# Kernel tuning notes

Hardware: AMD Instinct MI355X
Metric: run time of the kernel (lower is better)

The kernel has to match this reference:

```python
import jax, jax.numpy as jnp
import numpy as np

N_ENT, N_USR, C, E, NNZ, NREL, NHOPS = 150000, 60000, 64, 1000000, 1000000, 10, 2
EPS = 1e-12  # torch F.normalize default eps


def setup_inputs() -> dict:
    key = jax.random.key(0)
    ks = jax.random.split(key, 8)
    return {
        "user_emb": jax.random.normal(ks[0], (N_USR, C), dtype=jnp.float32),
        "entity_emb": jax.random.normal(ks[1], (N_ENT, C), dtype=jnp.float32),
        "weight": jax.random.normal(ks[2], (NREL - 1, C), dtype=jnp.float32) * 0.1,  # xavier-ish
        "inter_vals": jax.random.uniform(ks[3], (NNZ,), dtype=jnp.float32),
        "edge_index": jax.random.randint(ks[4], (2, E), 0, N_ENT),
        "edge_type": jax.random.randint(ks[5], (E,), 0, NREL - 1),
        "inter_rows": jax.random.randint(ks[6], (NNZ,), 0, N_USR),
        "inter_cols": jax.random.randint(ks[7], (NNZ,), 0, N_ENT),
    }


def _l2_normalize(x):
    n = jnp.sqrt(jnp.sum(x * x, axis=1, keepdims=True))
    return x / jnp.maximum(n, EPS)


def _hop(entity_emb, user_emb, head, tail, edge_type, weight,
         inter_rows, inter_cols, inter_vals):
    rel = weight[edge_type - 1]                      # [E, C]
    h = entity_emb[head]                             # [E, C]
    t = entity_emb[tail]                             # [E, C]
    neigh = t * rel                                  # [E, C]
    # calculate_sim_hrt: (||h*r||_2 * ||t*r||_2)^2, per-edge scalar
    hn = jnp.linalg.norm(h * rel, axis=1)            # [E]
    tn = jnp.linalg.norm(t * rel, axis=1)            # [E]
    att = (hn * tn) ** 2                             # [E]
    # scatter_softmax over groups of `head` (value identical across channels)
    m = jax.ops.segment_max(att, head, num_segments=N_ENT)
    e = jnp.exp(att - m[head])
    s = jax.ops.segment_sum(e, head, num_segments=N_ENT)
    w = e / s[head]                                  # [E]
    entity_agg = jax.ops.segment_sum(w[:, None] * neigh, head, num_segments=N_ENT)
    # entity_agg += interact_mat.T @ user_emb
    entity_agg = entity_agg + jax.ops.segment_sum(
        inter_vals[:, None] * user_emb[inter_rows], inter_cols, num_segments=N_ENT)
    # user_agg = interact_mat @ entity_emb
    user_agg = jax.ops.segment_sum(
        inter_vals[:, None] * entity_emb[inter_cols], inter_rows, num_segments=N_USR)
    return entity_agg, user_agg


def reference(user_emb, entity_emb, weight, inter_vals,
              edge_index, edge_type, inter_rows, inter_cols):
    head, tail = edge_index[0], edge_index[1]
    ent_res, usr_res = entity_emb, user_emb
    ent, usr = entity_emb, user_emb
    for _ in range(NHOPS):
        ent, usr = _hop(ent, usr, head, tail, edge_type, weight,
                        inter_rows, inter_cols, inter_vals)
        ent = _l2_normalize(ent)  # mess_dropout disabled (eval path)
        usr = _l2_normalize(usr)
        ent_res = ent_res + ent
        usr_res = usr_res + usr
    return ent_res, usr_res
```

## Files before the change

### kernel.cpp

```cpp
#include <hip/hip_runtime.h>
#include <hip/hip_fp16.h>
#include <math.h>

#define N_ENT  150000
#define N_USR  60000
#define CDIM   64
#define NE     1000000
#define NNZV   1000000
#define NREL9  9
#define NTOT   (2 * N_ENT + N_USR)
#define TOTAL_ITEMS (NE + 2 * NNZV)
#define SCAN_B ((NTOT + 1023) / 1024)

#define NXCD   8
#define H_PER  (N_ENT / NXCD)
#define R_PER  (N_USR / NXCD)
#define EPB    2048
#define NCHUNK ((NE + EPB - 1) / EPB)
#define HISTB  (NCHUNK * NXCD)

#define EG (N_ENT / 4)
#define UG (N_USR / 4)
#define UCVT ((N_USR * CDIM / 2 + 255) / 256)

template <int CTRL>
__device__ __forceinline__ float dpp_addf(float v) {
    int iv = __float_as_int(v);
    int x = __builtin_amdgcn_update_dpp(iv, iv, CTRL, 0xF, 0xF, true);
    return v + __int_as_float(x);
}
template <int CTRL>
__device__ __forceinline__ float dpp_maxf(float v) {
    int iv = __float_as_int(v);
    int x = __builtin_amdgcn_update_dpp(iv, iv, CTRL, 0xF, 0xF, true);
    return fmaxf(v, __int_as_float(x));
}
__device__ __forceinline__ float wave_sum(float v) {
    v = dpp_addf<0x111>(v);
    v = dpp_addf<0x112>(v);
    v = dpp_addf<0x114>(v);
    v = dpp_addf<0x118>(v);
    v = dpp_addf<0x142>(v);
    v = dpp_addf<0x143>(v);
    return __int_as_float(__builtin_amdgcn_readlane(__float_as_int(v), 63));
}
__device__ __forceinline__ float wave_max(float v) {
    v = dpp_maxf<0x111>(v);
    v = dpp_maxf<0x112>(v);
    v = dpp_maxf<0x114>(v);
    v = dpp_maxf<0x118>(v);
    v = dpp_maxf<0x142>(v);
    v = dpp_maxf<0x143>(v);
    return __int_as_float(__builtin_amdgcn_readlane(__float_as_int(v), 63));
}

__device__ __forceinline__ float bcast_f(float v, int l) { return __int_as_float(__builtin_amdgcn_readlane(__float_as_int(v), l)); }

__device__ __forceinline__ int block_excl_scan(int v, int* lds) {
    int lane = threadIdx.x & 63, wid = threadIdx.x >> 6;
    int incl = v;
#pragma unroll
    for (int o = 1; o < 64; o <<= 1) {
        int t = __shfl_up(incl, o, 64);
        if (lane >= o) incl += t;
    }
    if (lane == 63) lds[wid] = incl;
    __syncthreads();
    int nw = blockDim.x >> 6;
    if ((int)threadIdx.x < nw) {
        int s = lds[threadIdx.x];
        int si = s;
        for (int o = 1; o < nw; o <<= 1) {
            int t = __shfl_up(si, o, 64);
            if ((int)threadIdx.x >= o) si += t;
        }
        lds[threadIdx.x] = si - s;
    }
    __syncthreads();
    return incl - v + lds[wid];
}

__global__ __launch_bounds__(256) void k_histprep(
    const int* __restrict__ head, const int* __restrict__ cols,
    const int* __restrict__ rows, int* __restrict__ cnt,
    const float* __restrict__ ent, const float* __restrict__ usr,
    const float* __restrict__ wt,
    __half* __restrict__ ent16, __half* __restrict__ usr16,
    float* __restrict__ sq)
{
    int b = blockIdx.x;
    if (b < HISTB) {
        int role  = b & (NXCD - 1);
        int chunk = b >> 3;
        int h0 = role * H_PER, h1 = h0 + H_PER;
        int r0 = role * R_PER, r1 = r0 + R_PER;
        int base = chunk * EPB;
        int end  = min(base + EPB, NE);
        for (int i = base + (int)threadIdx.x; i < end; i += 256) {
            int h = head[i];
            int c = cols[i];
            int r = rows[i];
            if (h >= h0 && h < h1) atomicAdd(cnt + h, 1);
            if (c >= h0 && c < h1) atomicAdd(cnt + N_ENT + c, 1);
            if (r >= r0 && r < r1) atomicAdd(cnt + 2 * N_ENT + r, 1);
        }
    } else if (b < HISTB + EG) {
        int e = ((b - HISTB) * 256 + (int)threadIdx.x) >> 6;
        int lane = threadIdx.x & 63;
        float own = ent[(e << 6) + lane];
        ent16[(e << 6) + lane] = __float2half(own);
        float o2 = own * own;
        float mine = 0.f;
#pragma unroll
        for (int rt = 0; rt < NREL9; ++rt) {
            float r = wt[(rt << 6) + lane];
            float s = wave_sum(o2 * r * r);
            if (lane == rt) mine = s;
        }
        if (lane < NREL9) sq[e * NREL9 + lane] = mine;
    } else {
        int i = (b - HISTB - EG) * 256 + (int)threadIdx.x;
        if (i < N_USR * CDIM / 2) {
            float2 v = ((const float2*)usr)[i];
            ((__half2*)usr16)[i] = __floats2half2_rn(v.x, v.y);
        }
    }
}

__global__ __launch_bounds__(1024) void k_bsum(
    const int* __restrict__ cnt, int* __restrict__ bsum)
{
    __shared__ int lds[16];
    int i = blockIdx.x * 1024 + threadIdx.x;
    float v = (i < NTOT) ? (float)cnt[i] : 0.f;
    float s = wave_sum(v);
    int lane = threadIdx.x & 63, wid = threadIdx.x >> 6;
    if (lane == 0) lds[wid] = (int)s;
    __syncthreads();
    if (threadIdx.x == 0) {
        int t = 0;
        for (int k = 0; k < 16; ++k) t += lds[k];
        bsum[blockIdx.x] = t;
    }
}

__global__ __launch_bounds__(512) void k_scan_small(int* __restrict__ bsum)
{
    __shared__ int lds[16];
    int i = threadIdx.x;
    int v = (i < SCAN_B) ? bsum[i] : 0;
    int e = block_excl_scan(v, lds);
    if (i < SCAN_B) bsum[i] = e;
}

__global__ __launch_bounds__(1024) void k_scan_apply(
    const int* __restrict__ cnt, const int* __restrict__ bsum,
    int* __restrict__ start, int* __restrict__ cursor)
{
    __shared__ int lds[16];
    int i = blockIdx.x * 1024 + threadIdx.x;
    int v = (i < NTOT) ? cnt[i] : 0;
    int e = block_excl_scan(v, lds) + bsum[blockIdx.x];
    if (i < NTOT) { start[i] = e; cursor[i] = e; }
    else if (i == NTOT) { start[i] = TOTAL_ITEMS; }
}

__global__ __launch_bounds__(256) void k_scatter(
    const int* __restrict__ head, const int* __restrict__ tail,
    const int* __restrict__ etype,
    const int* __restrict__ rows, const int* __restrict__ cols,
    const float* __restrict__ vals,
    int* __restrict__ cursor,
    int* __restrict__ pk_h,
    int2* __restrict__ rc,
    int2* __restrict__ cv)
{
    int role  = blockIdx.x & (NXCD - 1);
    int chunk = blockIdx.x >> 3;
    int h0 = role * H_PER, h1 = h0 + H_PER;
    int r0 = role * R_PER, r1 = r0 + R_PER;
    int base = chunk * EPB;
    int end  = min(base + EPB, NE);
    for (int i = base + (int)threadIdx.x; i < end; i += 256) {
        int h = head[i];
        int c = cols[i];
        int r = rows[i];
        if (h >= h0 && h < h1) {
            int rt = etype[i] - 1;
            if (rt < 0) rt = 8;
            int p = atomicAdd(cursor + h, 1);
            if ((unsigned)p < (unsigned)NE) pk_h[p] = tail[i] | (rt << 18);
        }
        if (c >= h0 && c < h1) {
            int vb = __float_as_int(vals[i]);
            int p = atomicAdd(cursor + N_ENT + c, 1) - NE;
            if ((unsigned)p < (unsigned)NNZV) rc[p] = make_int2(r, vb);
        }
        if (r >= r0 && r < r1) {
            int vb = __float_as_int(vals[i]);
            int p = atomicAdd(cursor + 2 * N_ENT + r, 1) - 2 * NE;
            if ((unsigned)p < (unsigned)NNZV) cv[p] = make_int2(c, vb);
        }
    }
}

template <bool FIRST, bool LAST>
__global__ __launch_bounds__(256) void k_hop(
    const __half* __restrict__ ent16_cur, const __half* __restrict__ usr16_cur,
    const float* __restrict__ ent_res_base, const float* __restrict__ usr_res_base,
    const float* __restrict__ wt, const int* __restrict__ start,
    const int* __restrict__ pk_h, const float* __restrict__ sq_in,
    const int2* __restrict__ rc, const int2* __restrict__ cv,
    __half* __restrict__ ent16_next, __half* __restrict__ usr16_next,
    float* __restrict__ sq_out,
    float* __restrict__ out_ent, float* __restrict__ out_usr)
{
    int lane = threadIdx.x & 63;
    int b = blockIdx.x;

    if (b < EG) {
        int e = __builtin_amdgcn_readfirstlane((b * 256 + (int)threadIdx.x) >> 6);

        int s1 = min(start[e + 1], NE);
        int s0 = min(start[e], s1);
        float m = 0.f, l = 0.f, acc = 0.f;
        for (int base = s0; base < s1; base += 64) {
            int j = base + lane;
            int cnt = min(64, s1 - base);
            float att = 0.f;
            if (j < s1) {
                int pk = pk_h[j];
                int t = pk & 0x3FFFF, rt = (pk >> 18) & 15;
                att = sq_in[e * NREL9 + rt] * sq_in[t * NREL9 + rt];
            }
            float mn = fmaxf(m, wave_max(att));
            float scale = __expf(m - mn);
            float p = (j < s1) ? __expf(att - mn) : 0.f;
            l = l * scale + wave_sum(p);
            acc *= scale;
            m = mn;
            int k = 0;
            for (; k + 4 <= cnt; k += 4) {
#pragma unroll
                for (int q = 0; q < 4; ++q) {
                    int pkk = pk_h[base + k + q];
                    float wk = bcast_f(p, k + q);
                    const __half* tp = ent16_cur + ((pkk & 0x3FFFF) << 6);
                    const float*  wp = wt + (((pkk >> 18) & 15) << 6);
                    acc += wk * __half2float(tp[lane]) * wp[lane];
                }
            }
            for (; k < cnt; ++k) {
                int pkk = pk_h[base + k];
                float wk = bcast_f(p, k);
                const __half* tp = ent16_cur + ((pkk & 0x3FFFF) << 6);
                const float*  wp = wt + (((pkk >> 18) & 15) << 6);
                acc += wk * __half2float(tp[lane]) * wp[lane];
            }
        }
        float agg = (l > 0.f) ? acc / l : 0.f;

        int c1 = min(start[N_ENT + e + 1] - NE, NNZV);
        int c0 = max(min(start[N_ENT + e] - NE, c1), 0);
        {
            int k = c0;
            for (; k + 4 <= c1; k += 4) {
#pragma unroll
                for (int q = 0; q < 4; ++q) {
                    int2 t2 = rc[k + q];
                    agg += __int_as_float(t2.y) *
                           __half2float(usr16_cur[(t2.x << 6) + lane]);
                }
            }
            for (; k < c1; ++k) {
                int2 t2 = rc[k];
                agg += __int_as_float(t2.y) *
                       __half2float(usr16_cur[(t2.x << 6) + lane]);
            }
        }

        float s = wave_sum(agg * agg);
        float y = agg / fmaxf(sqrtf(s), 1e-12f);
        int oi = (e << 6) + lane;
        if (!LAST) {
            ent16_next[oi] = __float2half(y);
            float y2 = y * y;
            float mine = 0.f;
#pragma unroll
            for (int rt = 0; rt < NREL9; ++rt) {
                float r = wt[(rt << 6) + lane];
                float sv = wave_sum(y2 * r * r);
                if (lane == rt) mine = sv;
            }
            if (lane < NREL9) sq_out[e * NREL9 + lane] = mine;
        }
        if (FIRST) out_ent[oi] = ent_res_base[oi] + y;
        else       out_ent[oi] += y;
    } else {
        int u = __builtin_amdgcn_readfirstlane(((b - EG) * 256 + (int)threadIdx.x) >> 6);
        int s1 = min(start[2 * N_ENT + u + 1] - 2 * NE, NNZV);
        int s0 = max(min(start[2 * N_ENT + u] - 2 * NE, s1), 0);
        float accA = 0.f, accB = 0.f;
        {
            int k = s0;
            for (; k + 4 <= s1; k += 4) {
#pragma unroll
                for (int q = 0; q < 4; ++q) {
                    int2 t2 = cv[k + q];
                    float prod = __int_as_float(t2.y) *
                                 __half2float(ent16_cur[(t2.x << 6) + lane]);
                    if (q & 1) accB += prod; else accA += prod;
                }
            }
            for (; k < s1; ++k) {
                int2 t2 = cv[k];
                accA += __int_as_float(t2.y) *
                        __half2float(ent16_cur[(t2.x << 6) + lane]);
            }
        }
        float acc = accA + accB;
        float s = wave_sum(acc * acc);
        float y = acc / fmaxf(sqrtf(s), 1e-12f);
        int oi = (u << 6) + lane;
        if (!LAST) usr16_next[oi] = __float2half(y);
        if (FIRST) out_usr[oi] = usr_res_base[oi] + y;
        else       out_usr[oi] += y;
    }
}

extern "C" void kernel_launch(void* const* d_in, const int* in_sizes, int n_in,
                              void* d_out, int out_size, void* d_ws, size_t ws_size,
                              hipStream_t stream)
{
    const float* user_emb   = (const float*)d_in[0];
    const float* entity_emb = (const float*)d_in[1];
    const float* wt         = (const float*)d_in[2];
    const float* inter_vals = (const float*)d_in[3];
    const int*   edge_index = (const int*)d_in[4];
    const int*   etype      = (const int*)d_in[5];
    const int*   inter_rows = (const int*)d_in[6];
    const int*   inter_cols = (const int*)d_in[7];
    const int* head  = edge_index;
    const int* tailp = edge_index + NE;

    __half* ent16_a = (__half*)d_ws;
    __half* ent16_b = ent16_a + (size_t)N_ENT * CDIM;
    __half* usr16_a = ent16_b + (size_t)N_ENT * CDIM;
    __half* usr16_b = usr16_a + (size_t)N_USR * CDIM;
    int2*  rc     = (int2*)(usr16_b + (size_t)N_USR * CDIM);
    int2*  cv     = rc + NNZV;
    int*   pk_h   = (int*)(cv + NNZV);
    int*   cnt    = pk_h + NE;
    int*   start  = cnt + NTOT;
    int*   cursor = start + NTOT + 1;
    int*   bsum   = cursor + NTOT + 1;
    float* sq_a   = (float*)(bsum + SCAN_B);
    float* sq_b   = sq_a + (size_t)N_ENT * NREL9;

    float* out_ent = (float*)d_out;
    float* out_usr = out_ent + (size_t)N_ENT * CDIM;

    hipMemsetAsync(cnt, 0, (size_t)NTOT * sizeof(int), stream);
    k_histprep<<<HISTB + EG + UCVT, 256, 0, stream>>>(
        head, inter_cols, inter_rows, cnt,
        entity_emb, user_emb, wt, ent16_a, usr16_a, sq_a);
    k_bsum<<<SCAN_B, 1024, 0, stream>>>(cnt, bsum);
    k_scan_small<<<1, 512, 0, stream>>>(bsum);
    k_scan_apply<<<SCAN_B, 1024, 0, stream>>>(cnt, bsum, start, cursor);
    k_scatter<<<NCHUNK * NXCD, 256, 0, stream>>>(
        head, tailp, etype, inter_rows, inter_cols, inter_vals,
        cursor, pk_h, rc, cv);

    k_hop<true, false><<<EG + UG, 256, 0, stream>>>(
        ent16_a, usr16_a, entity_emb, user_emb, wt, start, pk_h, sq_a, rc, cv,
        ent16_b, usr16_b, sq_b, out_ent, out_usr);

    k_hop<false, true><<<EG + UG, 256, 0, stream>>>(
        ent16_b, usr16_b, nullptr, nullptr, wt, start, pk_h, sq_b, rc, cv,
        nullptr, nullptr, nullptr, out_ent, out_usr);
}
```

Before: 673.4 us.

## Replace global-atomic histogram with LDS-privatized slice histograms and reduction

Counting of head, column and row keys moves from global atomics into per-block LDS histograms. Each block covers a 16K-key slice over one eighth of the edges and writes a private partial histogram. A following kernel sums the partials into the count array, alongside the existing fp16 conversion work, and the separate memset is no longer needed. This is meant to remove global atomic contention, at the cost of reading each key array many times (once per slice) and using extra scratch space aliased onto an fp16 buffer that is unused at that point.

```diff
diff --git a/kernel.cpp b/kernel.cpp
--- a/kernel.cpp
+++ b/kernel.cpp
@@ -17,11 +17,20 @@
 #define R_PER  (N_USR / NXCD)
 #define EPB    2048
 #define NCHUNK ((NE + EPB - 1) / EPB)
-#define HISTB  (NCHUNK * NXCD)
 
 #define EG (N_ENT / 4)
 #define UG (N_USR / 4)
 #define UCVT ((N_USR * CDIM / 2 + 255) / 256)
+
+#define SLICE_K 16384
+#define SH 10
+#define SC 10
+#define SR 4
+#define NSLICE (SH + SC + SR)
+#define ESPLIT 8
+#define ECH (NE / ESPLIT)
+#define HIST_BLKS (NSLICE * ESPLIT)
+#define RB ((NTOT + 255) / 256)
 
 template <int CTRL>
 __device__ __forceinline__ float dpp_addf(float v) {
@@ -80,32 +89,54 @@
     return incl - v + lds[wid];
 }
 
-__global__ __launch_bounds__(256) void k_histprep(
+__global__ __launch_bounds__(256) void k_hist_lds(
     const int* __restrict__ head, const int* __restrict__ cols,
-    const int* __restrict__ rows, int* __restrict__ cnt,
+    const int* __restrict__ rows, int* __restrict__ priv)
+{
+    __shared__ int h[SLICE_K];
+    int sid = blockIdx.x >> 3, chunk = blockIdx.x & (ESPLIT - 1);
+    const int* key; int k0;
+    if (sid < SH)            { key = head; k0 = sid * SLICE_K; }
+    else if (sid < SH + SC)  { key = cols; k0 = (sid - SH) * SLICE_K; }
+    else                     { key = rows; k0 = (sid - SH - SC) * SLICE_K; }
+    for (int t = threadIdx.x; t < SLICE_K; t += 256) h[t] = 0;
+    __syncthreads();
+    const int4* key4 = (const int4*)(key + chunk * ECH);
+    for (int i = threadIdx.x; i < ECH / 4; i += 256) {
+        int4 k4 = key4[i];
+        int a = k4.x - k0, b = k4.y - k0, c = k4.z - k0, d = k4.w - k0;
+        if ((unsigned)a < (unsigned)SLICE_K) atomicAdd(&h[a], 1);
+        if ((unsigned)b < (unsigned)SLICE_K) atomicAdd(&h[b], 1);
+        if ((unsigned)c < (unsigned)SLICE_K) atomicAdd(&h[c], 1);
+        if ((unsigned)d < (unsigned)SLICE_K) atomicAdd(&h[d], 1);
+    }
+    __syncthreads();
+    int* dst = priv + (size_t)blockIdx.x * SLICE_K;
+    for (int t = threadIdx.x; t < SLICE_K; t += 256) dst[t] = h[t];
+}
+
+__global__ __launch_bounds__(256) void k_prepreduce(
+    const int* __restrict__ priv, int* __restrict__ cnt,
     const float* __restrict__ ent, const float* __restrict__ usr,
     const float* __restrict__ wt,
     __half* __restrict__ ent16, __half* __restrict__ usr16,
     float* __restrict__ sq)
 {
     int b = blockIdx.x;
-    if (b < HISTB) {
-        int role  = b & (NXCD - 1);
-        int chunk = b >> 3;
-        int h0 = role * H_PER, h1 = h0 + H_PER;
-        int r0 = role * R_PER, r1 = r0 + R_PER;
-        int base = chunk * EPB;
-        int end  = min(base + EPB, NE);
-        for (int i = base + (int)threadIdx.x; i < end; i += 256) {
-            int h = head[i];
-            int c = cols[i];
-            int r = rows[i];
-            if (h >= h0 && h < h1) atomicAdd(cnt + h, 1);
-            if (c >= h0 && c < h1) atomicAdd(cnt + N_ENT + c, 1);
-            if (r >= r0 && r < r1) atomicAdd(cnt + 2 * N_ENT + r, 1);
-        }
-    } else if (b < HISTB + EG) {
-        int e = ((b - HISTB) * 256 + (int)threadIdx.x) >> 6;
+    if (b < RB) {
+        int i = b * 256 + (int)threadIdx.x;
+        if (i >= NTOT) return;
+        int sid, local;
+        if (i < N_ENT)          { sid = i >> 14;                    local = i & (SLICE_K - 1); }
+        else if (i < 2 * N_ENT) { int j = i - N_ENT;     sid = SH + (j >> 14);      local = j & (SLICE_K - 1); }
+        else                    { int j = i - 2 * N_ENT; sid = SH + SC + (j >> 14); local = j & (SLICE_K - 1); }
+        const int* p = priv + (size_t)(sid * ESPLIT) * SLICE_K + local;
+        int s = 0;
+#pragma unroll
+        for (int c = 0; c < ESPLIT; ++c) s += p[(size_t)c * SLICE_K];
+        cnt[i] = s;
+    } else if (b < RB + EG) {
+        int e = ((b - RB) * 256 + (int)threadIdx.x) >> 6;
         int lane = threadIdx.x & 63;
         float own = ent[(e << 6) + lane];
         ent16[(e << 6) + lane] = __float2half(own);
@@ -119,7 +150,7 @@
         }
         if (lane < NREL9) sq[e * NREL9 + lane] = mine;
     } else {
-        int i = (b - HISTB - EG) * 256 + (int)threadIdx.x;
+        int i = (b - RB - EG) * 256 + (int)threadIdx.x;
         if (i < N_USR * CDIM / 2) {
             float2 v = ((const float2*)usr)[i];
             ((__half2*)usr16)[i] = __floats2half2_rn(v.x, v.y);
@@ -356,14 +387,14 @@
     int*   bsum   = cursor + NTOT + 1;
     float* sq_a   = (float*)(bsum + SCAN_B);
     float* sq_b   = sq_a + (size_t)N_ENT * NREL9;
+    int* priv = (int*)ent16_b;
 
     float* out_ent = (float*)d_out;
     float* out_usr = out_ent + (size_t)N_ENT * CDIM;
 
-    hipMemsetAsync(cnt, 0, (size_t)NTOT * sizeof(int), stream);
-    k_histprep<<<HISTB + EG + UCVT, 256, 0, stream>>>(
-        head, inter_cols, inter_rows, cnt,
-        entity_emb, user_emb, wt, ent16_a, usr16_a, sq_a);
+    k_hist_lds<<<HIST_BLKS, 256, 0, stream>>>(head, inter_cols, inter_rows, priv);
+    k_prepreduce<<<RB + EG + UCVT, 256, 0, stream>>>(
+        priv, cnt, entity_emb, user_emb, wt, ent16_a, usr16_a, sq_a);
     k_bsum<<<SCAN_B, 1024, 0, stream>>>(cnt, bsum);
     k_scan_small<<<1, 512, 0, stream>>>(bsum);
     k_scan_apply<<<SCAN_B, 1024, 0, stream>>>(cnt, bsum, start, cursor);
```

Result: faster. 625.5 us (-7.1%).
